# Kernel optimization log

Measured on AMD Instinct MI355X. Metric: run time of the kernel, lower is better.

## Reference

```python
import jax, jax.numpy as jnp
import numpy as np

B, C, IN_LEN, OUT_LEN, E, TOP_K, N_I = 1, 8192, 512, 512, 8, 2, 16


def setup_inputs() -> dict:
    key = jax.random.key(0)
    ks = jax.random.split(key, 8)
    w = lambda k, shape, sc=0.02: jax.random.normal(k, shape, dtype=jnp.float32) * sc
    return {
        "x": jax.random.normal(ks[0], (B, C, IN_LEN), dtype=jnp.float32),
        "Ins_tk": jax.random.normal(ks[1], (B, N_I, OUT_LEN), dtype=jnp.float32),
        "gate_w": w(ks[2], (IN_LEN, E)),            # Gate: Linear(in_len, E, bias=False)
        "expert_w": w(ks[3], (E, IN_LEN, OUT_LEN)),  # per-expert Linear weight (transposed)
        "expert_b": jnp.zeros((E, OUT_LEN), dtype=jnp.float32),
        "gamma_w": w(ks[4], (E, OUT_LEN)),          # EiLM gamma_generator: Linear(h,1,bias=False)
        "beta_w": w(ks[5], (E, OUT_LEN, OUT_LEN)),  # EiLM beta_generator (transposed)
        "rmod_w": w(ks[6], (OUT_LEN, E)),           # router_modulator: Linear(out_len, E, bias=False)
    }


def reference(x, Ins_tk, gate_w, expert_w, expert_b, gamma_w, beta_w, rmod_w):
    Bx, Cx, L = x.shape
    xf = x.reshape(-1, L)                                   # [N, in_len], N = B*C
    ins = Ins_tk[0]                                         # [N_i, out_len] (B==1 asserted)

    # Router: logits + expert-wise modulation of logits
    router_gamma = jnp.mean(ins @ rmod_w, axis=0)           # [E]
    logits = xf @ gate_w + router_gamma                     # [N, E]
    probs = jax.nn.softmax(logits.astype(jnp.float32), axis=-1)
    rw, sel = jax.lax.top_k(probs, TOP_K)                   # [N, k] values/indices (no renorm)

    # Combine weights per token per expert: sum_k rw[t,k] * onehot(sel[t,k])
    combine = jnp.sum(jax.nn.one_hot(sel, E, dtype=rw.dtype) * rw[..., None], axis=1)  # [N, E]

    # EiLM per-expert affine params: scalar gamma, vector beta (mean over instruction tokens)
    gam = jnp.mean(ins @ gamma_w.T, axis=0)                 # [E]
    bet = jnp.einsum('nh,ehd->ed', ins, beta_w) / N_I       # [E, out_len]

    # Per-expert linear over all tokens, then EiLM modulation
    eo = jnp.einsum('nl,eld->end', xf, expert_w) + expert_b[:, None, :]   # [E, N, out]
    mod = gam[:, None, None] * eo + bet[:, None, :]                        # [E, N, out]

    out = jnp.einsum('ne,end->nd', combine, mod)            # [N, out]
    return out.reshape(Bx, Cx, OUT_LEN)
```

## Files before the change

### kernel.cpp

```cpp
#include <hip/hip_runtime.h>
#include <hip/hip_bf16.h>

#define N_TOK 8192
#define INL   512
#define OUTL  512
#define NE    8
#define NI    16
#define EOFF  (OUTL * INL)

typedef unsigned short ushort_t;
typedef unsigned int   uint_t;
typedef short  short8  __attribute__((ext_vector_type(8)));
typedef float  floatx4 __attribute__((ext_vector_type(4)));

#define WS_GAM    2048u
#define WS_RGAM   2080u
#define WS_BET    2112u
#define WS_SELE   18496u
#define WS_SELW   51264u
#define WS_WT     182336u

__device__ __forceinline__ ushort_t f2bf(float f) {
    uint_t b = __float_as_uint(f);
    return (ushort_t)((b + 0x7FFFu + ((b >> 16) & 1u)) >> 16);
}
__device__ __forceinline__ uint_t pkbf(float a, float b) {
    __hip_bfloat162 h = __float22bfloat162_rn(make_float2(a, b));
    union { __hip_bfloat162 h2; uint_t u; } cv;
    cv.h2 = h;
    return cv.u;
}
__device__ __forceinline__ void dma16(const ushort_t* g, ushort_t* l) {
    __builtin_amdgcn_global_load_lds(
        (const __attribute__((address_space(1))) void*)g,
        (__attribute__((address_space(3))) void*)l,
        16, 0, 0);
}

__global__ __launch_bounds__(256)
void k_prep(const float* __restrict__ ins,
            const float* __restrict__ expert_w,
            const float* __restrict__ expert_b,
            const float* __restrict__ gamma_w,
            const float* __restrict__ beta_w,
            const float* __restrict__ rmod_w,
            ushort_t* __restrict__ wt,
            float* __restrict__ wsBet,
            float* __restrict__ wsGam, float* __restrict__ wsRgam) {
    __shared__ __align__(16) char smem[17152];
    int bx = blockIdx.x;
    int tid = threadIdx.x;

    if (bx < 512) {
        float (*tile)[65] = (float(*)[65])smem;
        int e = bx >> 6, rem = bx & 63;
        int lt = (rem >> 3) * 64, dt = (rem & 7) * 64;
        int dIdx = tid & 63, lq = tid >> 6;
        for (int i = 0; i < 16; ++i) {
            int l = lq * 16 + i;
            tile[l][dIdx] = expert_w[(e * INL + lt + l) * OUTL + dt + dIdx];
        }
        __syncthreads();
        int lIdx = tid & 63, dq = tid >> 6;
        for (int i = 0; i < 16; ++i) {
            int d = dq * 16 + i;
            wt[(e * OUTL + dt + d) * INL + lt + lIdx] = f2bf(tile[lIdx][d]);
        }
        return;
    }

    if (bx < 640) {
        float* sS  = (float*)smem;
        float* red = sS + 512;
        float* gamS = red + 256;
        int b2 = bx - 512;
        int e = b2 >> 4, dBase = (b2 & 15) * 32;
        for (int h = tid; h < INL; h += 256) {
            float a = 0.f;
            for (int n = 0; n < NI; ++n) a += ins[n * INL + h];
            sS[h] = a;
        }
        __syncthreads();
        if (tid < 64) {
            float g = 0.f;
            for (int j = 0; j < 8; ++j) g += sS[tid * 8 + j] * gamma_w[e * INL + tid * 8 + j];
            for (int off = 32; off >= 1; off >>= 1) g += __shfl_xor(g, off, 64);
            if (tid == 0) gamS[0] = g * (1.f / NI);
        }
        int doff = tid & 31, hq = tid >> 5;
        float a = 0.f;
        for (int j = 0; j < 64; ++j) {
            int h = hq * 64 + j;
            a += sS[h] * beta_w[(e * INL + h) * OUTL + dBase + doff];
        }
        red[tid] = a;
        __syncthreads();
        if (tid < 32) {
            float t = 0.f;
            for (int k = 0; k < 8; ++k) t += red[k * 32 + tid];
            int d = dBase + tid;
            wsBet[e * OUTL + d] = t * (1.f / NI) + gamS[0] * expert_b[e * OUTL + d];
        }
        return;
    }

    {
        float* sS = (float*)smem;
        float* pg = sS + 512;
        float* pr = pg + 64;
        for (int h = tid; h < INL; h += 256) {
            float a = 0.f;
            for (int n = 0; n < NI; ++n) a += ins[n * INL + h];
            sS[h] = a;
        }
        __syncthreads();
        if (tid < 64) {
            int e = tid & 7, qq = tid >> 3;
            float g = 0.f, r = 0.f;
            for (int j = 0; j < 64; ++j) {
                int h = qq * 64 + j;
                float sv = sS[h];
                g += sv * gamma_w[e * INL + h];
                r += sv * rmod_w[h * NE + e];
            }
            pg[tid] = g; pr[tid] = r;
        }
        __syncthreads();
        if (tid < NE) {
            float g = 0.f, r = 0.f;
            for (int qq = 0; qq < 8; ++qq) { g += pg[qq * 8 + tid]; r += pr[qq * 8 + tid]; }
            wsGam[tid]  = g * (1.f / NI);
            wsRgam[tid] = r * (1.f / NI);
        }
    }
}

__global__ void k_route(const float* __restrict__ x,
                        const float* __restrict__ gate_w,
                        const float* __restrict__ wsGam,
                        const float* __restrict__ wsRgam,
                        int* __restrict__ selE, float4* __restrict__ selW) {
    __shared__ float gateT[NE * INL];
    int tid = threadIdx.x;
    for (int i = 0; i < 16; ++i) {
        int f = tid + 256 * i;
        float v = gate_w[f];
        gateT[(f & 7) * INL + (f >> 3)] = v;
    }
    __syncthreads();

    int w = tid >> 6, lane = tid & 63;
    int tbase = blockIdx.x * 16 + w * 4;

    for (int tt = 0; tt < 4; ++tt) {
        int t = tbase + tt;
        float2 xv[4];
        for (int i = 0; i < 4; ++i)
            xv[i] = *(const float2*)(x + (size_t)t * INL + 2 * lane + 128 * i);

        float acc[NE];
        for (int e = 0; e < NE; ++e) acc[e] = 0.f;
        for (int i = 0; i < 4; ++i) {
            int c = 2 * lane + 128 * i;
            for (int e = 0; e < NE; ++e)
                acc[e] += xv[i].x * gateT[e * INL + c] + xv[i].y * gateT[e * INL + c + 1];
        }
        for (int e = 0; e < NE; ++e) {
            float a = acc[e];
            for (int off = 32; off >= 1; off >>= 1) a += __shfl_xor(a, off, 64);
            acc[e] = a;
        }
        float logit[NE];
        for (int e = 0; e < NE; ++e) logit[e] = acc[e] + wsRgam[e];

        int i0 = 0; float m0 = logit[0];
        for (int e = 1; e < NE; ++e) if (logit[e] > m0) { m0 = logit[e]; i0 = e; }
        int i1 = -1; float m1 = -3.4e38f;
        for (int e = 0; e < NE; ++e) if (e != i0 && logit[e] > m1) { m1 = logit[e]; i1 = e; }

        float S = 0.f;
        for (int e = 0; e < NE; ++e) S += expf(logit[e] - m0);
        float rw0 = 1.0f / S;
        float rw1 = expf(m1 - m0) / S;

        if (lane == 0) {
            selE[t] = i0 | (i1 << 8);
            selW[t] = make_float4(rw0 * wsGam[i0], rw1 * wsGam[i1], rw0, rw1);
        }
    }
}

__global__ __launch_bounds__(256, 4)
void k_gemm(const float* __restrict__ x, const ushort_t* __restrict__ wt,
            const int* __restrict__ selE, const float4* __restrict__ selW,
            const float* __restrict__ wsBet, float* __restrict__ out) {
    int bx = blockIdx.x;
    int rt = bx & 127;
    int ct = bx >> 7;
    __shared__ ushort_t Blds[2][64 * 64];

    int tid = threadIdx.x;
    int wid = tid >> 6, lane = tid & 63;
    int wm = wid * 16;
    int mrow = lane & 15, laneq = lane >> 4, q8 = laneq * 8, qr = laneq * 4;

    int tokL = rt * 64 + wm + mrow;
    float wv[NE];
    {
        int es = selE[tokL];
        float4 w4 = selW[tokL];
        int e0 = es & 255, e1 = es >> 8;
        for (int e = 0; e < NE; ++e)
            wv[e] = (e == e0) ? w4.x : ((e == e1) ? w4.y : 0.f);
    }
    const float* arowp = x + (size_t)tokL * INL + q8;

    int c0 = tid, c1 = tid + 256;
    int col0 = c0 >> 3, kg0 = ((c0 & 7) - col0) & 7;
    int col1 = c1 >> 3, kg1 = ((c1 & 7) - col1) & 7;
    const ushort_t* pB0 = wt + (size_t)(ct * 64 + col0) * INL + kg0 * 8;
    const ushort_t* pB1 = wt + (size_t)(ct * 64 + col1) * INL + kg1 * 8;
    ushort_t* ldsW0 = &Blds[0][0] + (wid * 64) * 8;
    ushort_t* ldsW1 = &Blds[0][0] + (256 + wid * 64) * 8;

    int fcol[4], frot0[4];
    for (int nt = 0; nt < 4; ++nt) {
        fcol[nt] = nt * 16 + mrow;
        frot0[nt] = (laneq + fcol[nt]) & 7;
    }

    floatx4 comb[4];
    for (int nt = 0; nt < 4; ++nt) comb[nt] = (floatx4){0.f, 0.f, 0.f, 0.f};

    dma16(pB0, ldsW0);
    dma16(pB1, ldsW1);
    __syncthreads();

    float4 ar[2][2];

    #pragma unroll 1
    for (int kc = 0; kc < 8; ++kc) {
        for (int ks = 0; ks < 2; ++ks) {
            const float* p = arowp + kc * 64 + ks * 32;
            ar[ks][0] = *(const float4*)p;
            ar[ks][1] = *(const float4*)(p + 4);
        }

        #pragma unroll
        for (int e = 0; e < NE; ++e) {
            int step = kc * 8 + e;
            int buf = step & 1;
            int ne = e + 1, nkc = kc;
            if (ne == NE) { ne = 0; nkc = kc + 1; }
            if (nkc < 8) {
                size_t off = (size_t)ne * EOFF + (size_t)nkc * 64;
                int nb = (step + 1) & 1;
                dma16(pB0 + off, ldsW0 + nb * 4096);
                dma16(pB1 + off, ldsW1 + nb * 4096);
            }

            const ushort_t* B = &Blds[buf][0];
            short8 bf[4][2];
            for (int nt = 0; nt < 4; ++nt) {
                int cb = fcol[nt] * 64;
                bf[nt][0] = *(const short8*)&B[cb + frot0[nt] * 8];
                bf[nt][1] = *(const short8*)&B[cb + ((frot0[nt] + 4) & 7) * 8];
            }
            float w = wv[e];
            for (int ks = 0; ks < 2; ++ks) {
                union { uint4 u; short8 s; } af;
                float4 a0 = ar[ks][0], a1 = ar[ks][1];
                af.u.x = pkbf(a0.x * w, a0.y * w);
                af.u.y = pkbf(a0.z * w, a0.w * w);
                af.u.z = pkbf(a1.x * w, a1.y * w);
                af.u.w = pkbf(a1.z * w, a1.w * w);
                for (int nt = 0; nt < 4; ++nt)
                    comb[nt] = __builtin_amdgcn_mfma_f32_16x16x32_bf16(
                        af.s, bf[nt][ks], comb[nt], 0, 0, 0);
            }
            __syncthreads();
        }
    }

    for (int ri = 0; ri < 4; ++ri) {
        int row = wm + qr + ri;
        int tok = rt * 64 + row;
        int es = selE[tok];
        float4 w4 = selW[tok];
        int e0 = es & 255, e1 = es >> 8;
        for (int nt = 0; nt < 4; ++nt) {
            int col = ct * 64 + nt * 16 + mrow;
            float bet = w4.z * wsBet[e0 * OUTL + col] + w4.w * wsBet[e1 * OUTL + col];
            out[(size_t)tok * OUTL + col] = comb[nt][ri] + bet;
        }
    }
}

extern "C" void kernel_launch(void* const* d_in, const int* in_sizes, int n_in,
                              void* d_out, int out_size, void* d_ws, size_t ws_size,
                              hipStream_t stream) {
    const float* x        = (const float*)d_in[0];
    const float* ins      = (const float*)d_in[1];
    const float* gate_w   = (const float*)d_in[2];
    const float* expert_w = (const float*)d_in[3];
    const float* expert_b = (const float*)d_in[4];
    const float* gamma_w  = (const float*)d_in[5];
    const float* beta_w   = (const float*)d_in[6];
    const float* rmod_w   = (const float*)d_in[7];
    float* out = (float*)d_out;

    char* ws = (char*)d_ws;
    float*    wsGam  = (float*)(ws + WS_GAM);
    float*    wsRgam = (float*)(ws + WS_RGAM);
    float*    wsBet  = (float*)(ws + WS_BET);
    int*      selE   = (int*)(ws + WS_SELE);
    float4*   selW   = (float4*)(ws + WS_SELW);
    ushort_t* wt     = (ushort_t*)(ws + WS_WT);

    k_prep<<<641, 256, 0, stream>>>(ins, expert_w, expert_b,
                                    gamma_w, beta_w, rmod_w,
                                    wt, wsBet, wsGam, wsRgam);
    k_route<<<N_TOK / 16, 256, 0, stream>>>(x, gate_w, wsGam, wsRgam, selE, selW);
    k_gemm<<<1024, 256, 0, stream>>>(x, wt, selE, selW, wsBet, out);
}
```

Baseline: 150.8 us.

## Apply routing weights to per-expert MFMA outputs and split weight transpose kernel

The GEMM now converts each x tile to bf16 once per k-chunk instead of rescaling and re-packing it by the routing weight for every expert. It computes per-expert partial products from zero and accumulates them into the output with fp32 per-row weight FMAs, which cuts the packing ALU work in the inner loop but adds 16 FMAs per expert step and more registers. The expert-weight transpose moves to its own kernel that uses float4 loads and packed 16-byte bf16 stores, and the stats and beta work become a separate, smaller kernel. This adds one more kernel launch.

Result: slower. 270.4 us (+79.3%).

```diff
diff --git a/kernel.cpp b/kernel.cpp
--- a/kernel.cpp
+++ b/kernel.cpp
@@ -20,10 +20,6 @@
 #define WS_SELW   51264u
 #define WS_WT     182336u
 
-__device__ __forceinline__ ushort_t f2bf(float f) {
-    uint_t b = __float_as_uint(f);
-    return (ushort_t)((b + 0x7FFFu + ((b >> 16) & 1u)) >> 16);
-}
 __device__ __forceinline__ uint_t pkbf(float a, float b) {
     __hip_bfloat162 h = __float22bfloat162_rn(make_float2(a, b));
     union { __hip_bfloat162 h2; uint_t u; } cv;
@@ -38,54 +34,32 @@
 }
 
 __global__ __launch_bounds__(256)
-void k_prep(const float* __restrict__ ins,
-            const float* __restrict__ expert_w,
-            const float* __restrict__ expert_b,
-            const float* __restrict__ gamma_w,
-            const float* __restrict__ beta_w,
-            const float* __restrict__ rmod_w,
-            ushort_t* __restrict__ wt,
-            float* __restrict__ wsBet,
-            float* __restrict__ wsGam, float* __restrict__ wsRgam) {
-    __shared__ __align__(16) char smem[17152];
-    int bx = blockIdx.x;
-    int tid = threadIdx.x;
-
-    if (bx < 512) {
-        float (*tile)[65] = (float(*)[65])smem;
-        int e = bx >> 6, rem = bx & 63;
-        int lt = (rem >> 3) * 64, dt = (rem & 7) * 64;
-        int dIdx = tid & 63, lq = tid >> 6;
-        for (int i = 0; i < 16; ++i) {
-            int l = lq * 16 + i;
-            tile[l][dIdx] = expert_w[(e * INL + lt + l) * OUTL + dt + dIdx];
-        }
-        __syncthreads();
-        int lIdx = tid & 63, dq = tid >> 6;
-        for (int i = 0; i < 16; ++i) {
-            int d = dq * 16 + i;
-            wt[(e * OUTL + dt + d) * INL + lt + lIdx] = f2bf(tile[lIdx][d]);
-        }
-        return;
-    }
-
-    if (bx < 640) {
-        float* sS  = (float*)smem;
-        float* red = sS + 512;
-        float* gamS = red + 256;
-        int b2 = bx - 512;
-        int e = b2 >> 4, dBase = (b2 & 15) * 32;
-        for (int h = tid; h < INL; h += 256) {
-            float a = 0.f;
-            for (int n = 0; n < NI; ++n) a += ins[n * INL + h];
-            sS[h] = a;
-        }
-        __syncthreads();
+void k_betstats(const float* __restrict__ ins,
+                const float* __restrict__ gamma_w,
+                const float* __restrict__ rmod_w,
+                const float* __restrict__ beta_w,
+                const float* __restrict__ expert_b,
+                float* __restrict__ wsBet,
+                float* __restrict__ wsGam, float* __restrict__ wsRgam) {
+    __shared__ float sS[INL];
+    __shared__ float red[256];
+    __shared__ float aux[1];
+    int bx = blockIdx.x, tid = threadIdx.x;
+
+    for (int h = tid; h < INL; h += 256) {
+        float a = 0.f;
+        for (int n = 0; n < NI; ++n) a += ins[n * INL + h];
+        sS[h] = a;
+    }
+    __syncthreads();
+
+    if (bx < 128) {
+        int e = bx >> 4, dBase = (bx & 15) * 32;
         if (tid < 64) {
             float g = 0.f;
             for (int j = 0; j < 8; ++j) g += sS[tid * 8 + j] * gamma_w[e * INL + tid * 8 + j];
             for (int off = 32; off >= 1; off >>= 1) g += __shfl_xor(g, off, 64);
-            if (tid == 0) gamS[0] = g * (1.f / NI);
+            if (tid == 0) aux[0] = g * (1.f / NI);
         }
         int doff = tid & 31, hq = tid >> 5;
         float a = 0.f;
@@ -99,39 +73,28 @@
             float t = 0.f;
             for (int k = 0; k < 8; ++k) t += red[k * 32 + tid];
             int d = dBase + tid;
-            wsBet[e * OUTL + d] = t * (1.f / NI) + gamS[0] * expert_b[e * OUTL + d];
+            wsBet[e * OUTL + d] = t * (1.f / NI) + aux[0] * expert_b[e * OUTL + d];
         }
         return;
     }
 
-    {
-        float* sS = (float*)smem;
-        float* pg = sS + 512;
-        float* pr = pg + 64;
-        for (int h = tid; h < INL; h += 256) {
-            float a = 0.f;
-            for (int n = 0; n < NI; ++n) a += ins[n * INL + h];
-            sS[h] = a;
-        }
-        __syncthreads();
-        if (tid < 64) {
-            int e = tid & 7, qq = tid >> 3;
-            float g = 0.f, r = 0.f;
-            for (int j = 0; j < 64; ++j) {
-                int h = qq * 64 + j;
-                float sv = sS[h];
-                g += sv * gamma_w[e * INL + h];
-                r += sv * rmod_w[h * NE + e];
-            }
-            pg[tid] = g; pr[tid] = r;
-        }
-        __syncthreads();
-        if (tid < NE) {
-            float g = 0.f, r = 0.f;
-            for (int qq = 0; qq < 8; ++qq) { g += pg[qq * 8 + tid]; r += pr[qq * 8 + tid]; }
-            wsGam[tid]  = g * (1.f / NI);
-            wsRgam[tid] = r * (1.f / NI);
-        }
+    if (tid < 64) {
+        int e = tid & 7, qq = tid >> 3;
+        float g = 0.f, r = 0.f;
+        for (int j = 0; j < 64; ++j) {
+            int h = qq * 64 + j;
+            float sv = sS[h];
+            g += sv * gamma_w[e * INL + h];
+            r += sv * rmod_w[h * NE + e];
+        }
+        red[tid] = g; red[64 + tid] = r;
+    }
+    __syncthreads();
+    if (tid < NE) {
+        float g = 0.f, r = 0.f;
+        for (int qq = 0; qq < 8; ++qq) { g += red[qq * 8 + tid]; r += red[64 + qq * 8 + tid]; }
+        wsGam[tid]  = g * (1.f / NI);
+        wsRgam[tid] = r * (1.f / NI);
     }
 }
 
@@ -190,6 +153,35 @@
     }
 }
 
+__global__ __launch_bounds__(256)
+void k_wt(const float* __restrict__ expert_w, ushort_t* __restrict__ wt) {
+    __shared__ float tile[64][65];
+    int bx = blockIdx.x;
+    int e = bx >> 6, rem = bx & 63;
+    int lt = (rem >> 3) * 64, dt = (rem & 7) * 64;
+    int tid = threadIdx.x;
+
+    int lr = tid >> 4, dc = (tid & 15) * 4;
+    for (int p = 0; p < 4; ++p) {
+        int l = p * 16 + lr;
+        float4 v = *(const float4*)(expert_w + (size_t)(e * INL + lt + l) * OUTL + dt + dc);
+        tile[l][dc] = v.x; tile[l][dc + 1] = v.y;
+        tile[l][dc + 2] = v.z; tile[l][dc + 3] = v.w;
+    }
+    __syncthreads();
+
+    for (int i = 0; i < 2; ++i) {
+        int ch = tid + i * 256;
+        int d = ch >> 3, lc = ch & 7;
+        uint4 o;
+        o.x = pkbf(tile[lc * 8 + 0][d], tile[lc * 8 + 1][d]);
+        o.y = pkbf(tile[lc * 8 + 2][d], tile[lc * 8 + 3][d]);
+        o.z = pkbf(tile[lc * 8 + 4][d], tile[lc * 8 + 5][d]);
+        o.w = pkbf(tile[lc * 8 + 6][d], tile[lc * 8 + 7][d]);
+        *(uint4*)(wt + (size_t)(e * OUTL + dt + d) * INL + lt + lc * 8) = o;
+    }
+}
+
 __global__ __launch_bounds__(256, 4)
 void k_gemm(const float* __restrict__ x, const ushort_t* __restrict__ wt,
             const int* __restrict__ selE, const float4* __restrict__ selW,
@@ -204,16 +196,16 @@
     int wm = wid * 16;
     int mrow = lane & 15, laneq = lane >> 4, q8 = laneq * 8, qr = laneq * 4;
 
-    int tokL = rt * 64 + wm + mrow;
-    float wv[NE];
-    {
-        int es = selE[tokL];
-        float4 w4 = selW[tokL];
+    float wv4[4][NE];
+    for (int ri = 0; ri < 4; ++ri) {
+        int tok = rt * 64 + wm + qr + ri;
+        int es = selE[tok];
+        float4 w4 = selW[tok];
         int e0 = es & 255, e1 = es >> 8;
         for (int e = 0; e < NE; ++e)
-            wv[e] = (e == e0) ? w4.x : ((e == e1) ? w4.y : 0.f);
-    }
-    const float* arowp = x + (size_t)tokL * INL + q8;
+            wv4[ri][e] = (e == e0) ? w4.x : ((e == e1) ? w4.y : 0.f);
+    }
+    const float* arowp = x + (size_t)(rt * 64 + wm + mrow) * INL + q8;
 
     int c0 = tid, c1 = tid + 256;
     int col0 = c0 >> 3, kg0 = ((c0 & 7) - col0) & 7;
@@ -231,19 +223,23 @@
 
     floatx4 comb[4];
     for (int nt = 0; nt < 4; ++nt) comb[nt] = (floatx4){0.f, 0.f, 0.f, 0.f};
+    const floatx4 zf = (floatx4){0.f, 0.f, 0.f, 0.f};
 
     dma16(pB0, ldsW0);
     dma16(pB1, ldsW1);
     __syncthreads();
 
-    float4 ar[2][2];
-
     #pragma unroll 1
     for (int kc = 0; kc < 8; ++kc) {
+        union { uint4 u; short8 s; } af[2];
         for (int ks = 0; ks < 2; ++ks) {
             const float* p = arowp + kc * 64 + ks * 32;
-            ar[ks][0] = *(const float4*)p;
-            ar[ks][1] = *(const float4*)(p + 4);
+            float4 a0 = *(const float4*)p;
+            float4 a1 = *(const float4*)(p + 4);
+            af[ks].u.x = pkbf(a0.x, a0.y);
+            af[ks].u.y = pkbf(a0.z, a0.w);
+            af[ks].u.z = pkbf(a1.x, a1.y);
+            af[ks].u.w = pkbf(a1.z, a1.w);
         }
 
         #pragma unroll
@@ -260,24 +256,17 @@
             }
 
             const ushort_t* B = &Blds[buf][0];
-            short8 bf[4][2];
+            floatx4 acc[4];
             for (int nt = 0; nt < 4; ++nt) {
                 int cb = fcol[nt] * 64;
-                bf[nt][0] = *(const short8*)&B[cb + frot0[nt] * 8];
-                bf[nt][1] = *(const short8*)&B[cb + ((frot0[nt] + 4) & 7) * 8];
+                short8 b0 = *(const short8*)&B[cb + frot0[nt] * 8];
+                short8 b1 = *(const short8*)&B[cb + ((frot0[nt] + 4) & 7) * 8];
+                acc[nt] = __builtin_amdgcn_mfma_f32_16x16x32_bf16(af[0].s, b0, zf, 0, 0, 0);
+                acc[nt] = __builtin_amdgcn_mfma_f32_16x16x32_bf16(af[1].s, b1, acc[nt], 0, 0, 0);
             }
-            float w = wv[e];
-            for (int ks = 0; ks < 2; ++ks) {
-                union { uint4 u; short8 s; } af;
-                float4 a0 = ar[ks][0], a1 = ar[ks][1];
-                af.u.x = pkbf(a0.x * w, a0.y * w);
-                af.u.y = pkbf(a0.z * w, a0.w * w);
-                af.u.z = pkbf(a1.x * w, a1.y * w);
-                af.u.w = pkbf(a1.z * w, a1.w * w);
-                for (int nt = 0; nt < 4; ++nt)
-                    comb[nt] = __builtin_amdgcn_mfma_f32_16x16x32_bf16(
-                        af.s, bf[nt][ks], comb[nt], 0, 0, 0);
-            }
+            for (int nt = 0; nt < 4; ++nt)
+                for (int ri = 0; ri < 4; ++ri)
+                    comb[nt][ri] += wv4[ri][e] * acc[nt][ri];
             __syncthreads();
         }
     }
@@ -317,9 +306,9 @@
     float4*   selW   = (float4*)(ws + WS_SELW);
     ushort_t* wt     = (ushort_t*)(ws + WS_WT);
 
-    k_prep<<<641, 256, 0, stream>>>(ins, expert_w, expert_b,
-                                    gamma_w, beta_w, rmod_w,
-                                    wt, wsBet, wsGam, wsRgam);
+    k_betstats<<<129, 256, 0, stream>>>(ins, gamma_w, rmod_w, beta_w, expert_b,
+                                        wsBet, wsGam, wsRgam);
     k_route<<<N_TOK / 16, 256, 0, stream>>>(x, gate_w, wsGam, wsRgam, selE, selW);
+    k_wt<<<512, 256, 0, stream>>>(expert_w, wt);
     k_gemm<<<1024, 256, 0, stream>>>(x, wt, selE, selW, wsBet, out);
 }
```
